# Performance work log

Measured on AMD Instinct MI355X. Metric: run time of the kernel, lower is better.

## Reference

```python
import jax, jax.numpy as jnp
import numpy as np

CNN_DIM = 256
CLASS_NUM = 6
NHOPS = 2
ATT_DIM = 50


def conv1d(x, w, b, pad):
    # x: [B, Cin, L], w: [Cout, Cin, K]
    y = jax.lax.conv_general_dilated(x, w, (1,), [(pad, pad)],
                                     dimension_numbers=('NCH', 'OIH', 'NCH'))
    return y + b[None, :, None]


def setup_inputs() -> dict:
    key = jax.random.key(0)
    ks = jax.random.split(key, 16)
    B, L, V, GE, DE = 8, 128, 30000, 300, 100
    IN = GE + DE
    C = CLASS_NUM
    s = 0.02
    inp = {}
    inp['x'] = jax.random.randint(ks[0], (B, L), 0, V)
    inp['x_len'] = L  # python int, stands in for x_len[0] (max length)
    inp['x_mask'] = jnp.ones((B, L), dtype=jnp.float32)
    inp['gen_table'] = jax.random.normal(ks[1], (V, GE), jnp.float32) * s
    inp['domain_table'] = jax.random.normal(ks[2], (V, DE), jnp.float32) * s
    inp['w1'] = jax.random.normal(ks[3], (128, IN, 5)) * s
    inp['b1'] = jnp.zeros((128,))
    inp['w2'] = jax.random.normal(ks[4], (128, IN, 3)) * s
    inp['b2'] = jnp.zeros((128,))
    inp['w3'] = jax.random.normal(ks[5], (256, 256, 5)) * s
    inp['b3'] = jnp.zeros((256,))
    inp['w4'] = jax.random.normal(ks[6], (256, 256, 5)) * s
    inp['b4'] = jnp.zeros((256,))
    inp['w5'] = jax.random.normal(ks[7], (256, 256, 5)) * s
    inp['b5'] = jnp.zeros((256,))
    inp['wq'] = jax.random.normal(ks[8], (CNN_DIM, ATT_DIM)) * s
    inp['bq'] = jnp.zeros((ATT_DIM,))
    inp['wv'] = jax.random.normal(ks[9], (CNN_DIM, ATT_DIM)) * s
    inp['bv'] = jnp.zeros((ATT_DIM,))
    inp['vv'] = jax.random.normal(ks[10], (ATT_DIM,)) * s
    inp['wf'] = jax.random.normal(ks[11], (2 * CNN_DIM + 3 * C, 2 * CNN_DIM)) * s
    inp['bf'] = jnp.zeros((2 * CNN_DIM,))
    inp['wc'] = jax.random.normal(ks[12], (2 * CNN_DIM, C)) * s
    inp['bc'] = jnp.zeros((C,))
    return inp


def reference(x, x_len, x_mask, gen_table, domain_table,
              w1, b1, w2, b2, w3, b3, w4, b4, w5, b5,
              wq, bq, wv, bv, vv, wf, bf, wc, bc):
    # embeddings (dropout omitted: eval mode)
    emb = jnp.concatenate([gen_table[x], domain_table[x]], axis=2)  # [B,L,400]
    xe = jnp.swapaxes(emb, 1, 2)  # [B,400,L]
    xc = jax.nn.relu(jnp.concatenate([conv1d(xe, w1, b1, 2),
                                      conv1d(xe, w2, b2, 1)], axis=1))
    xc = jax.nn.relu(conv1d(xc, w3, b3, 2))
    xc = jax.nn.relu(conv1d(xc, w4, b4, 2))
    xc = jax.nn.relu(conv1d(xc, w5, b5, 2))
    xc = jnp.swapaxes(xc, 1, 2)[:, :x_len, :]  # [B,L,256]
    mask = x_mask[:, :x_len]
    # perceptron (additive) self-attention: v^T tanh(Wq q_i + Wv v_j)
    q = xc @ wq + bq  # [B,L,50]
    v = xc @ wv + bv  # [B,L,50]
    scores = jnp.tanh(q[:, :, None, :] + v[:, None, :, :]) @ vv  # [B,L,L]
    scores = jnp.where(mask[:, None, :] == 0, -1e9, scores)
    attn = jax.nn.softmax(scores, axis=2)
    merged = jnp.einsum('bij,bjd->bid', attn, xc) * mask[:, :, None]
    xc = xc + merged
    B, L, D = xc.shape
    # grid features: (i,j) -> [h_i, h_j]
    features = jnp.concatenate([
        jnp.broadcast_to(xc[:, :, None, :], (B, L, L, D)),
        jnp.broadcast_to(xc[:, None, :, :], (B, L, L, D))], axis=3)  # [B,L,L,512]
    # upper-triangular validity mask on the grid
    m2 = jnp.triu(mask[:, None, :] * mask[:, :, None])[..., None]  # [B,L,L,1]
    logits = features @ wc + bc  # [B,L,L,C]
    for _ in range(NHOPS):
        probs = logits
        lg = probs * m2
        lm = jnp.maximum(jnp.max(lg, axis=1), jnp.max(lg, axis=2))  # [B,L,C]
        row = jnp.broadcast_to(lm[:, :, None, :], (B, L, L, lm.shape[-1]))
        grid = jnp.concatenate([row, jnp.swapaxes(row, 1, 2)], axis=3)  # [B,L,L,2C]
        features = jnp.concatenate([features, grid, probs], axis=3) @ wf + bf
        logits = features @ wc + bc
    return logits
```

## Files before the change

### kernel.cpp

```cpp
#include <hip/hip_runtime.h>
#include <math.h>

#define LSEQ 128
#define BB 8
#define M_TOK (BB*LSEQ)

typedef __attribute__((ext_vector_type(8))) short short8;
typedef __attribute__((ext_vector_type(4))) float floatx4;

__device__ __forceinline__ unsigned short bf16_rne(float v) {
    union { float f; unsigned u; } a; a.f = v;
    return (unsigned short)((a.u + 0x7fffu + ((a.u >> 16) & 1u)) >> 16);
}
__device__ __forceinline__ float bf16_to_f(unsigned short h) {
    union { unsigned u; float f; } b; b.u = ((unsigned)h) << 16;
    return b.f;
}
__device__ __forceinline__ void split2(float v, unsigned short& h, unsigned short& l) {
    h = bf16_rne(v);
    l = bf16_rne(v - bf16_to_f(h));
}

struct PreArgs {
    const float *w1, *w2, *w3, *w4, *w5;
    unsigned short *B1h, *B1l, *B2h, *B2l, *B3h, *B3l, *B4h, *B4l, *B5h, *B5l;
    const int* x;
    const float* gen;
    const float* dom;
    unsigned short *Eh, *El;
    const float* wf;
    const float* wc;
    float* Wfc;
};
__global__ __launch_bounds__(256) void stage_kernel(PreArgs a) {
    int y = blockIdx.y;
    int tid = threadIdx.x;
    if (y < 3) {
        const float* w = (y == 0) ? a.w3 : (y == 1) ? a.w4 : a.w5;
        unsigned short* dh = (y == 0) ? a.B3h : (y == 1) ? a.B4h : a.B5h;
        unsigned short* dl = (y == 0) ? a.B3l : (y == 1) ? a.B4l : a.B5l;
        int idx = blockIdx.x * 256 + tid;
        int j = idx & 7;
        int n = (idx >> 3) & 255;
        int g = idx >> 11;
        int cg = g & 31, kk = g >> 5;
        int ci = cg * 8 + j;
        float v = w[(n * 256 + ci) * 5 + kk];
        unsigned short h, l; split2(v, h, l);
        dh[idx] = h; dl[idx] = l;
    } else if (y == 3) {
        int idx = blockIdx.x * 256 + tid;
        if (idx >= 5 * 52 * 128 * 8) return;
        int j = idx & 7;
        int n = (idx >> 3) & 127;
        int g = idx >> 10;
        int cg = g % 52, kk = g / 52;
        int ci = cg * 8 + j;
        float v = (ci < 400) ? a.w1[(n * 400 + ci) * 5 + kk] : 0.f;
        unsigned short h, l; split2(v, h, l);
        a.B1h[idx] = h; a.B1l[idx] = l;
    } else if (y == 4) {
        int idx = blockIdx.x * 256 + tid;
        if (idx >= 3 * 52 * 128 * 8) return;
        int j = idx & 7;
        int n = (idx >> 3) & 127;
        int g = idx >> 10;
        int cg = g % 52, kk = g / 52;
        int ci = cg * 8 + j;
        float v = (ci < 400) ? a.w2[(n * 400 + ci) * 3 + kk] : 0.f;
        unsigned short h, l; split2(v, h, l);
        a.B2h[idx] = h; a.B2l[idx] = l;
    } else if (y == 5) {
        int m = blockIdx.x;
        if (m >= M_TOK) return;
        int t = a.x[m];
        for (int c = tid; c < 416; c += 256) {
            float v = (c < 300) ? a.gen[t * 300 + c]
                    : (c < 400) ? a.dom[t * 100 + (c - 300)] : 0.f;
            unsigned short h, l; split2(v, h, l);
            a.Eh[m * 416 + c] = h;
            a.El[m * 416 + c] = l;
        }
    } else {
        int r = blockIdx.x;
        if (r >= 512 || tid >= 64) return;
        int l = tid;
        float p[6] = {0,0,0,0,0,0};
        const float* row = a.wf + r * 512;
        #pragma unroll
        for (int k = 0; k < 8; ++k) {
            int n = l + 64 * k;
            float v = row[n];
            #pragma unroll
            for (int c = 0; c < 6; ++c) p[c] += v * a.wc[n * 6 + c];
        }
        #pragma unroll
        for (int c = 0; c < 6; ++c)
            for (int off = 32; off >= 1; off >>= 1) p[c] += __shfl_xor(p[c], off, 64);
        if (l == 0) {
            #pragma unroll
            for (int c = 0; c < 6; ++c) a.Wfc[r * 6 + c] = p[c];
        }
    }
}

__global__ __launch_bounds__(256) void conv1_mfma(
        const unsigned short* __restrict__ Eh, const unsigned short* __restrict__ El,
        const unsigned short* __restrict__ B1h, const unsigned short* __restrict__ B1l,
        const unsigned short* __restrict__ B2h, const unsigned short* __restrict__ B2l,
        const float* __restrict__ b1, const float* __restrict__ b2,
        unsigned short* __restrict__ Xoh, unsigned short* __restrict__ Xol,
        const float* __restrict__ wf, const float* __restrict__ bf,
        const float* __restrict__ wc, const float* __restrict__ Wfc,
        float* __restrict__ U) {
    __shared__ __align__(16) unsigned short xsh[20 * 424];
    __shared__ __align__(16) unsigned short xsl[20 * 424];
    int by = blockIdx.y;
    int tid = threadIdx.x;
    if (by == 4) {
        if (tid >= 64) return;
        int l = tid;
        for (int i = 0; i < 9; ++i) {
            int r = blockIdx.x + 64 * i;
            if (r >= 531) break;
            const float* row = (r < 530) ? (wf + r * 512) : bf;
            float p[12];
            #pragma unroll
            for (int c = 0; c < 12; ++c) p[c] = 0.f;
            #pragma unroll
            for (int k = 0; k < 8; ++k) {
                int n = l + 64 * k;
                float v = row[n];
                #pragma unroll
                for (int c = 0; c < 6; ++c) {
                    p[c]     += v * wc[n * 6 + c];
                    p[c + 6] += v * Wfc[n * 6 + c];
                }
            }
            #pragma unroll
            for (int c = 0; c < 12; ++c)
                for (int off = 32; off >= 1; off >>= 1) p[c] += __shfl_xor(p[c], off, 64);
            if (l == 0) {
                #pragma unroll
                for (int c = 0; c < 12; ++c) U[r * 12 + c] = p[c];
            }
        }
        return;
    }
    int mt = blockIdx.x;
    int p0 = mt * 16;
    int b = p0 >> 7, l0 = p0 & 127;
    for (int i = tid; i < 2 * 1040; i += 256) {
        int sel = i >= 1040;
        int u2 = sel ? i - 1040 : i;
        int j = u2 / 52, cg = u2 % 52;
        int l = l0 - 2 + j;
        short8 v = {0,0,0,0,0,0,0,0};
        if (l >= 0 && l < 128) {
            const unsigned short* src = (sel ? El : Eh) + (b * 128 + l) * 416 + cg * 8;
            v = *(const short8*)src;
        }
        *(short8*)((sel ? xsl : xsh) + j * 424 + cg * 8) = v;
    }
    __syncthreads();
    int w = tid >> 6, lane = tid & 63;
    int m = lane & 15, q = lane >> 4;
    bool br2 = (by >= 2);
    int n0b = (by & 1) * 64;
    int nB = n0b + w * 16 + m;
    floatx4 acc0 = {0,0,0,0}, acc1 = {0,0,0,0}, acc2 = {0,0,0,0};
    if (!br2) {
        for (int kk = 0; kk < 5; ++kk) {
            const unsigned short* arh = xsh + (m + kk) * 424;
            const unsigned short* arl = xsl + (m + kk) * 424;
            #pragma unroll
            for (int u = 0; u < 13; ++u) {
                short8 ah = *(const short8*)(arh + u * 32 + q * 8);
                short8 al = *(const short8*)(arl + u * 32 + q * 8);
                int boff = (((kk * 52 + u * 4 + q) * 128) + nB) * 8;
                short8 bh = *(const short8*)(B1h + boff);
                short8 bl = *(const short8*)(B1l + boff);
                acc0 = __builtin_amdgcn_mfma_f32_16x16x32_bf16(ah, bh, acc0, 0, 0, 0);
                acc1 = __builtin_amdgcn_mfma_f32_16x16x32_bf16(ah, bl, acc1, 0, 0, 0);
                acc2 = __builtin_amdgcn_mfma_f32_16x16x32_bf16(al, bh, acc2, 0, 0, 0);
            }
        }
    } else {
        for (int kk = 0; kk < 3; ++kk) {
            const unsigned short* arh = xsh + (m + kk + 1) * 424;
            const unsigned short* arl = xsl + (m + kk + 1) * 424;
            #pragma unroll
            for (int u = 0; u < 13; ++u) {
                short8 ah = *(const short8*)(arh + u * 32 + q * 8);
                short8 al = *(const short8*)(arl + u * 32 + q * 8);
                int boff = (((kk * 52 + u * 4 + q) * 128) + nB) * 8;
                short8 bh = *(const short8*)(B2h + boff);
                short8 bl = *(const short8*)(B2l + boff);
                acc0 = __builtin_amdgcn_mfma_f32_16x16x32_bf16(ah, bh, acc0, 0, 0, 0);
                acc1 = __builtin_amdgcn_mfma_f32_16x16x32_bf16(ah, bl, acc1, 0, 0, 0);
                acc2 = __builtin_amdgcn_mfma_f32_16x16x32_bf16(al, bh, acc2, 0, 0, 0);
            }
        }
    }
    __syncthreads();
    float* fl = (float*)xsh;
    #pragma unroll
    for (int reg = 0; reg < 4; ++reg)
        fl[(q * 4 + reg) * 68 + w * 16 + m] = acc0[reg] + acc1[reg] + acc2[reg];
    __syncthreads();
    int ocb = br2 ? 128 + n0b : n0b;
    const float* bias = br2 ? b2 : b1;
    #pragma unroll
    for (int i = 0; i < 4; ++i) {
        int e = tid + 256 * i;
        int mm = e >> 6, nn = e & 63;
        float val = fl[mm * 68 + nn] + bias[n0b + nn];
        val = fmaxf(val, 0.f);
        unsigned short h, l; split2(val, h, l);
        int o = (p0 + mm) * 256 + ocb + nn;
        Xoh[o] = h; Xol[o] = l;
    }
}

__global__ __launch_bounds__(256) void conv256_mfma(
        const unsigned short* __restrict__ Xih, const unsigned short* __restrict__ Xil,
        const unsigned short* __restrict__ Bh, const unsigned short* __restrict__ Bl,
        const float* __restrict__ bias, int outmode,
        unsigned short* __restrict__ Xoh, unsigned short* __restrict__ Xol,
        float* __restrict__ fout) {
    __shared__ __align__(16) unsigned short xsh[20 * 264];
    __shared__ __align__(16) unsigned short xsl[20 * 264];
    int mt = blockIdx.x;
    int p0 = mt * 16;
    int b = p0 >> 7, l0 = p0 & 127;
    int n0 = blockIdx.y * 64;
    int tid = threadIdx.x;
    for (int i = tid; i < 2 * 640; i += 256) {
        int sel = i >= 640;
        int u2 = sel ? i - 640 : i;
        int j = u2 >> 5, cg = u2 & 31;
        int l = l0 - 2 + j;
        short8 v = {0,0,0,0,0,0,0,0};
        if (l >= 0 && l < 128) {
            const unsigned short* src = (sel ? Xil : Xih) + (b * 128 + l) * 256 + cg * 8;
            v = *(const short8*)src;
        }
        *(short8*)((sel ? xsl : xsh) + j * 264 + cg * 8) = v;
    }
    __syncthreads();
    int w = tid >> 6, lane = tid & 63;
    int m = lane & 15, q = lane >> 4;
    int nB = n0 + w * 16 + m;
    floatx4 acc0 = {0,0,0,0}, acc1 = {0,0,0,0}, acc2 = {0,0,0,0};
    for (int kk = 0; kk < 5; ++kk) {
        const unsigned short* arh = xsh + (m + kk) * 264;
        const unsigned short* arl = xsl + (m + kk) * 264;
        #pragma unroll
        for (int u = 0; u < 8; ++u) {
            short8 ah = *(const short8*)(arh + u * 32 + q * 8);
            short8 al = *(const short8*)(arl + u * 32 + q * 8);
            int boff = (((kk * 32 + u * 4 + q) * 256) + nB) * 8;
            short8 bh = *(const short8*)(Bh + boff);
            short8 bl = *(const short8*)(Bl + boff);
            acc0 = __builtin_amdgcn_mfma_f32_16x16x32_bf16(ah, bh, acc0, 0, 0, 0);
        acc1 = __builtin_amdgcn_mfma_f32_16x16x32_bf16(ah, bl, acc1, 0, 0, 0);
            acc2 = __builtin_amdgcn_mfma_f32_16x16x32_bf16(al, bh, acc2, 0, 0, 0);
        }
    }
    __syncthreads();
    float* fl = (float*)xsh;
    #pragma unroll
    for (int reg = 0; reg < 4; ++reg)
        fl[(q * 4 + reg) * 68 + w * 16 + m] = acc0[reg] + acc1[reg] + acc2[reg];
    __syncthreads();
    #pragma unroll
    for (int i = 0; i < 4; ++i) {
        int e = tid + 256 * i;
        int mm = e >> 6, nn = e & 63;
        float val = fl[mm * 68 + nn] + bias[n0 + nn];
        val = fmaxf(val, 0.f);
        int o = (p0 + mm) * 256 + n0 + nn;
        if (outmode == 0) {
            unsigned short h, l; split2(val, h, l);
            Xoh[o] = h; Xol[o] = l;
        } else {
            fout[o] = val;
        }
    }
}

__global__ __launch_bounds__(128) void qv_v2(const float* __restrict__ xc,
        const float* __restrict__ wq, const float* __restrict__ bq,
        const float* __restrict__ wv, const float* __restrict__ bv,
        float* __restrict__ q, float* __restrict__ v) {
    int m = blockIdx.x;
    int tid = threadIdx.x;
    int w = tid >> 6, d = tid & 63;
    if (d >= 50) return;
    const float* W = w ? wv : wq;
    float a = w ? bv[d] : bq[d];
    const float* xm = xc + m * 256;
    #pragma unroll 8
    for (int c = 0; c < 256; ++c) a += xm[c] * W[c * 50 + d];
    (w ? v : q)[m * 50 + d] = a;
}

__global__ __launch_bounds__(256) void attn_v2(const float* __restrict__ xc,
        const float* __restrict__ q, const float* __restrict__ v,
        const float* __restrict__ vv, const float* __restrict__ xmask,
        const float* __restrict__ wc, const float* __restrict__ bc,
        float* __restrict__ xc2, float* __restrict__ f0, float* __restrict__ g0) {
    __shared__ float vs[128 * 50];
    __shared__ float spart[128], aarr[128], xrow[256], qrow[52], vvs[52], red[4];
    int bi = blockIdx.x;
    int b = bi >> 7;
    int tid = threadIdx.x;
    for (int idx = tid; idx < 128 * 50; idx += 256) vs[idx] = v[b * 6400 + idx];
    if (tid < 50) { qrow[tid] = q[bi * 50 + tid]; vvs[tid] = vv[tid]; }
    __syncthreads();
    int j = tid & 127, half = tid >> 7;
    int d0 = half * 25;
    const float* vj = vs + j * 50 + d0;
    float s = 0.f;
    #pragma unroll
    for (int d = 0; d < 25; ++d) {
        float x = qrow[d0 + d] + vj[d];
        float e = __expf(2.f * x);
        s += (1.f - 2.f / (e + 1.f)) * vvs[d0 + d];
    }
    if (half) spart[j] = s;
    __syncthreads();
    float stot = 0.f;
    if (!half) {
        stot = s + spart[j];
        if (xmask[b * LSEQ + j] == 0.f) stot = -1e9f;
    }
    if (tid < 128) {
        float m = stot;
        #pragma unroll
        for (int off = 32; off >= 1; off >>= 1) m = fmaxf(m, __shfl_xor(m, off, 64));
        if ((tid & 63) == 0) red[tid >> 6] = m;
    }
    __syncthreads();
    float mx = fmaxf(red[0], red[1]);
    float e = 0.f;
    if (tid < 128) {
        e = __expf(stot - mx);
        float su = e;
        #pragma unroll
        for (int off = 32; off >= 1; off >>= 1) su += __shfl_xor(su, off, 64);
        if ((tid & 63) == 0) red[2 + (tid >> 6)] = su;
    }
    __syncthreads();
    float denom = red[2] + red[3];
    if (tid < 128) aarr[j] = e / denom;
    __syncthreads();
    float maskI = xmask[bi];
    const float* xcb = xc + b * LSEQ * 256;
    float acc = 0.f;
    #pragma unroll 8
    for (int jj = 0; jj < 128; ++jj) acc += aarr[jj] * xcb[jj * 256 + tid];
    float val = xc[bi * 256 + tid] + acc * maskI;
    xc2[bi * 256 + tid] = val;
    xrow[tid] = val;
    __syncthreads();
    int grp = tid >> 4, l16 = tid & 15;
    if (grp < 12) {
        int c = grp % 6, gsel = grp / 6;
        const float* wcc = wc + gsel * 256 * 6 + c;
        float a = 0.f;
        #pragma unroll
        for (int ch = l16; ch < 256; ch += 16) a += xrow[ch] * wcc[ch * 6];
        #pragma unroll
        for (int off = 8; off >= 1; off >>= 1) a += __shfl_down(a, off, 16);
        if (l16 == 0) {
            if (gsel == 0) f0[bi * 6 + c] = a + bc[c];
            else           g0[bi * 6 + c] = a;
        }
    }
}

__global__ __launch_bounds__(128) void lm_scan_v3(const float* __restrict__ f,
        const float* __restrict__ g, int stride, float* __restrict__ lm) {
    __shared__ float sf[128], sg[128];
    int bc = blockIdx.x;
    int b = bc / 6, c = bc - b * 6;
    int p = threadIdx.x;
    float fv = f[(b * LSEQ + p) * stride + c];
    float gv = g[(b * LSEQ + p) * stride + c];
    sf[p] = fv; sg[p] = gv;
    __syncthreads();
    float pf = fv, sgx = gv;
    #pragma unroll
    for (int off = 1; off < 128; off <<= 1) {
        float a = (p >= off) ? sf[p - off] : -INFINITY;
        float d = (p + off < 128) ? sg[p + off] : -INFINITY;
        __syncthreads();
        pf = fmaxf(pf, a); sgx = fmaxf(sgx, d);
        sf[p] = pf; sg[p] = sgx;
        __syncthreads();
    }
    float M1 = pf + gv;
    if (p < LSEQ - 1) M1 = fmaxf(M1, 0.f);
    float M2 = fv + sgx;
    if (p > 0) M2 = fmaxf(M2, 0.f);
    lm[(b * LSEQ + p) * 6 + c] = fmaxf(M1, M2);
}

__global__ __launch_bounds__(64) void hopfold_kernel(const float* __restrict__ xc2,
        const float* __restrict__ U, const float* __restrict__ lm0,
        const float* __restrict__ f0, const float* __restrict__ g0,
        const float* __restrict__ bc,
        float* __restrict__ outF, float* __restrict__ outG) {
    int m = blockIdx.x;
    int y = blockIdx.y;
    int tid = threadIdx.x;
    const float* Urows = U + (y ? 256 : 0) * 12;
    float p[12];
    #pragma unroll
    for (int c = 0; c < 12; ++c) p[c] = 0.f;
    for (int k = tid; k < 256; k += 64) {
        float a = xc2[m * 256 + k];
        const float* ur = Urows + k * 12;
        #pragma unroll
        for (int c = 0; c < 12; ++c) p[c] += a * ur[c];
    }
    #pragma unroll
    for (int c = 0; c < 12; ++c)
        for (int off = 32; off >= 1; off >>= 1) p[c] += __shfl_xor(p[c], off, 64);
    if (tid == 0) {
        const float* Bb = U + (y ? 518 : 512) * 12;
        const float* Db = U + 524 * 12;
        const float* fg = y ? g0 : f0;
        float* out = y ? outG : outF;
        float lmv[6], fgv[6];
        #pragma unroll
        for (int j = 0; j < 6; ++j) { lmv[j] = lm0[m * 6 + j]; fgv[j] = fg[m * 6 + j]; }
        #pragma unroll
        for (int c = 0; c < 12; ++c) {
            float s = p[c];
            #pragma unroll
            for (int j = 0; j < 6; ++j) s += lmv[j] * Bb[j * 12 + c] + fgv[j] * Db[j * 12 + c];
            if (!y) { s += U[530 * 12 + c]; if (c < 6) s += bc[c]; }
            out[m * 12 + c] = s;
        }
    }
}

__global__ __launch_bounds__(128) void f2g2_kernel(const float* __restrict__ f1phi,
        const float* __restrict__ g1gam, const float* __restrict__ lm1,
        const float* __restrict__ U, const float* __restrict__ bc,
        float* __restrict__ f2, float* __restrict__ g2) {
    __shared__ float Us[19 * 12], bcs[6];
    int tid = threadIdx.x;
    for (int i = tid; i < 19 * 12; i += 128) Us[i] = U[512 * 12 + i];
    if (tid < 6) bcs[tid] = bc[tid];
    __syncthreads();
    int m = blockIdx.x * 128 + tid;
    float lmv[6], f1v[6], g1v[6];
    #pragma unroll
    for (int j = 0; j < 6; ++j) {
        lmv[j] = lm1[m * 6 + j];
        f1v[j] = f1phi[m * 12 + j];
        g1v[j] = g1gam[m * 12 + j];
    }
    #pragma unroll
    for (int c = 0; c < 6; ++c) {
        float sf = f1phi[m * 12 + 6 + c] + Us[18 * 12 + c] + bcs[c];
        float sg = g1gam[m * 12 + 6 + c];
        #pragma unroll
        for (int j = 0; j < 6; ++j) {
            sf += lmv[j] * Us[j * 12 + c]       + f1v[j] * Us[(12 + j) * 12 + c];
            sg += lmv[j] * Us[(6 + j) * 12 + c] + g1v[j] * Us[(12 + j) * 12 + c];
        }
        f2[m * 6 + c] = sf;
        g2[m * 6 + c] = sg;
    }
}

__global__ __launch_bounds__(256) void writeout_kernel(const float* __restrict__ f2,
        const float* __restrict__ g2, float* __restrict__ out) {
    int idx = blockIdx.x * 256 + threadIdx.x;
    int c = idx % 6;
    int r = idx / 6;
    int j = r & 127;
    int bi = r >> 7;
    int b = bi >> 7;
    out[idx] = f2[bi * 6 + c] + g2[(b * LSEQ + j) * 6 + c];
}

extern "C" void kernel_launch(void* const* d_in, const int* in_sizes, int n_in,
                              void* d_out, int out_size, void* d_ws, size_t ws_size,
                              hipStream_t stream) {
    const int*   x     = (const int*)d_in[0];
    const float* xmask = (const float*)d_in[2];
    const float* gen   = (const float*)d_in[3];
    const float* dom   = (const float*)d_in[4];
    const float* w1    = (const float*)d_in[5];
    const float* b1    = (const float*)d_in[6];
    const float* w2    = (const float*)d_in[7];
    const float* b2    = (const float*)d_in[8];
    const float* w3    = (const float*)d_in[9];
    const float* b3    = (const float*)d_in[10];
    const float* w4    = (const float*)d_in[11];
    const float* b4    = (const float*)d_in[12];
    const float* w5    = (const float*)d_in[13];
    const float* b5    = (const float*)d_in[14];
    const float* wq    = (const float*)d_in[15];
    const float* bq    = (const float*)d_in[16];
    const float* wv    = (const float*)d_in[17];
    const float* bv    = (const float*)d_in[18];
    const float* vv    = (const float*)d_in[19];
    const float* wf    = (const float*)d_in[20];
    const float* bf    = (const float*)d_in[21];
    const float* wc    = (const float*)d_in[22];
    const float* bc    = (const float*)d_in[23];

    float* fb = (float*)d_ws;
    float* bufB  = fb;
    float* xc2   = bufB  + 262144;
    float* qb    = xc2   + 262144;
    float* vb    = qb    + 51200;
    float* Wfc   = vb    + 51200;
    float* U     = Wfc   + 3072;
    float* f0    = U     + 6376;
    float* g0    = f0    + 6144;
    float* lm0   = g0    + 6144;
    float* lm1   = lm0   + 6144;
    float* f1phi = lm1   + 6144;
    float* g1gam = f1phi + 12288;
    float* f2    = g1gam + 12288;
    float* g2    = f2    + 6144;
    unsigned short* sb = (unsigned short*)(g2 + 6144 + 32);
    unsigned short* Eh  = sb;             sb += 425984;
    unsigned short* El  = sb;             sb += 425984;
    unsigned short* B1h = sb;             sb += 266240;
    unsigned short* B1l = sb;             sb += 266240;
    unsigned short* B2h = sb;             sb += 159744;
    unsigned short* B2l = sb;             sb += 159744;
    unsigned short* B3h = sb;             sb += 327680;
    unsigned short* B3l = sb;             sb += 327680;
    unsigned short* B4h = sb;             sb += 327680;
    unsigned short* B4l = sb;             sb += 327680;
    unsigned short* B5h = sb;             sb += 327680;
    unsigned short* B5l = sb;             sb += 327680;
    unsigned short* X3h = sb;             sb += 262144;
    unsigned short* X3l = sb;             sb += 262144;
    unsigned short* X4h = sb;             sb += 262144;
    unsigned short* X4l = sb;             sb += 262144;

    PreArgs pa;
    pa.w1 = w1; pa.w2 = w2; pa.w3 = w3; pa.w4 = w4; pa.w5 = w5;
    pa.B1h = B1h; pa.B1l = B1l; pa.B2h = B2h; pa.B2l = B2l;
    pa.B3h = B3h; pa.B3l = B3l; pa.B4h = B4h; pa.B4l = B4l;
    pa.B5h = B5h; pa.B5l = B5l;
    pa.x = x; pa.gen = gen; pa.dom = dom; pa.Eh = Eh; pa.El = El;
    pa.wf = wf; pa.wc = wc; pa.Wfc = Wfc;
    stage_kernel<<<dim3(1280, 7), 256, 0, stream>>>(pa);

    conv1_mfma<<<dim3(64, 5), 256, 0, stream>>>(Eh, El, B1h, B1l, B2h, B2l, b1, b2,
                                                X3h, X3l, wf, bf, wc, Wfc, U);
    conv256_mfma<<<dim3(64, 4), 256, 0, stream>>>(X3h, X3l, B3h, B3l, b3, 0,
                                                  X4h, X4l, nullptr);
    conv256_mfma<<<dim3(64, 4), 256, 0, stream>>>(X4h, X4l, B4h, B4l, b4, 0,
                                                  X3h, X3l, nullptr);
    conv256_mfma<<<dim3(64, 4), 256, 0, stream>>>(X3h, X3l, B5h, B5l, b5, 1,
                                                  nullptr, nullptr, bufB);

    qv_v2<<<M_TOK, 128, 0, stream>>>(bufB, wq, bq, wv, bv, qb, vb);
    attn_v2<<<M_TOK, 256, 0, stream>>>(bufB, qb, vb, vv, xmask, wc, bc, xc2, f0, g0);

    lm_scan_v3<<<48, 128, 0, stream>>>(f0, g0, 6, lm0);
    hopfold_kernel<<<dim3(M_TOK, 2), 64, 0, stream>>>(xc2, U, lm0, f0, g0, bc, f1phi, g1gam);
    lm_scan_v3<<<48, 128, 0, stream>>>(f1phi, g1gam, 12, lm1);
    f2g2_kernel<<<8, 128, 0, stream>>>(f1phi, g1gam, lm1, U, bc, f2, g2);

    writeout_kernel<<<(BB*LSEQ*LSEQ*6)/256, 256, 0, stream>>>(f2, g2, (float*)d_out);
}
```

Before: 240.1 us.

## Fuse hop scans, folds and writeout into two kernels; enlarge conv M-tile

```diff
diff --git a/kernel.cpp b/kernel.cpp
--- a/kernel.cpp
+++ b/kernel.cpp
@@ -228,16 +228,16 @@
         const float* __restrict__ bias, int outmode,
         unsigned short* __restrict__ Xoh, unsigned short* __restrict__ Xol,
         float* __restrict__ fout) {
-    __shared__ __align__(16) unsigned short xsh[20 * 264];
-    __shared__ __align__(16) unsigned short xsl[20 * 264];
+    __shared__ __align__(16) unsigned short xsh[36 * 264];
+    __shared__ __align__(16) unsigned short xsl[36 * 264];
     int mt = blockIdx.x;
-    int p0 = mt * 16;
+    int p0 = mt * 32;
     int b = p0 >> 7, l0 = p0 & 127;
     int n0 = blockIdx.y * 64;
     int tid = threadIdx.x;
-    for (int i = tid; i < 2 * 640; i += 256) {
-        int sel = i >= 640;
-        int u2 = sel ? i - 640 : i;
+    for (int i = tid; i < 2 * 1152; i += 256) {
+        int sel = i >= 1152;
+        int u2 = sel ? i - 1152 : i;
         int j = u2 >> 5, cg = u2 & 31;
         int l = l0 - 2 + j;
         short8 v = {0,0,0,0,0,0,0,0};
@@ -251,30 +251,40 @@
     int w = tid >> 6, lane = tid & 63;
     int m = lane & 15, q = lane >> 4;
     int nB = n0 + w * 16 + m;
-    floatx4 acc0 = {0,0,0,0}, acc1 = {0,0,0,0}, acc2 = {0,0,0,0};
+    floatx4 acc0a = {0,0,0,0}, acc1a = {0,0,0,0}, acc2a = {0,0,0,0};
+    floatx4 acc0b = {0,0,0,0}, acc1b = {0,0,0,0}, acc2b = {0,0,0,0};
     for (int kk = 0; kk < 5; ++kk) {
-        const unsigned short* arh = xsh + (m + kk) * 264;
-        const unsigned short* arl = xsl + (m + kk) * 264;
+        const unsigned short* arh0 = xsh + (m + kk) * 264;
+        const unsigned short* arl0 = xsl + (m + kk) * 264;
+        const unsigned short* arh1 = arh0 + 16 * 264;
+        const unsigned short* arl1 = arl0 + 16 * 264;
         #pragma unroll
         for (int u = 0; u < 8; ++u) {
-            short8 ah = *(const short8*)(arh + u * 32 + q * 8);
-            short8 al = *(const short8*)(arl + u * 32 + q * 8);
+            short8 ah0 = *(const short8*)(arh0 + u * 32 + q * 8);
+            short8 al0 = *(const short8*)(arl0 + u * 32 + q * 8);
+            short8 ah1 = *(const short8*)(arh1 + u * 32 + q * 8);
+            short8 al1 = *(const short8*)(arl1 + u * 32 + q * 8);
             int boff = (((kk * 32 + u * 4 + q) * 256) + nB) * 8;
             short8 bh = *(const short8*)(Bh + boff);
             short8 bl = *(const short8*)(Bl + boff);
-            acc0 = __builtin_amdgcn_mfma_f32_16x16x32_bf16(ah, bh, acc0, 0, 0, 0);
-        acc1 = __builtin_amdgcn_mfma_f32_16x16x32_bf16(ah, bl, acc1, 0, 0, 0);
-            acc2 = __builtin_amdgcn_mfma_f32_16x16x32_bf16(al, bh, acc2, 0, 0, 0);
+            acc0a = __builtin_amdgcn_mfma_f32_16x16x32_bf16(ah0, bh, acc0a, 0, 0, 0);
+            acc1a = __builtin_amdgcn_mfma_f32_16x16x32_bf16(ah0, bl, acc1a, 0, 0, 0);
+            acc2a = __builtin_amdgcn_mfma_f32_16x16x32_bf16(al0, bh, acc2a, 0, 0, 0);
+            acc0b = __builtin_amdgcn_mfma_f32_16x16x32_bf16(ah1, bh, acc0b, 0, 0, 0);
+            acc1b = __builtin_amdgcn_mfma_f32_16x16x32_bf16(ah1, bl, acc1b, 0, 0, 0);
+            acc2b = __builtin_amdgcn_mfma_f32_16x16x32_bf16(al1, bh, acc2b, 0, 0, 0);
         }
     }
     __syncthreads();
     float* fl = (float*)xsh;
     #pragma unroll
-    for (int reg = 0; reg < 4; ++reg)
-        fl[(q * 4 + reg) * 68 + w * 16 + m] = acc0[reg] + acc1[reg] + acc2[reg];
-    __syncthreads();
-    #pragma unroll
-    for (int i = 0; i < 4; ++i) {
+    for (int reg = 0; reg < 4; ++reg) {
+        fl[(q * 4 + reg) * 68 + w * 16 + m]        = acc0a[reg] + acc1a[reg] + acc2a[reg];
+        fl[(16 + q * 4 + reg) * 68 + w * 16 + m]   = acc0b[reg] + acc1b[reg] + acc2b[reg];
+    }
+    __syncthreads();
+    #pragma unroll
+    for (int i = 0; i < 8; ++i) {
         int e = tid + 256 * i;
         int mm = e >> 6, nn = e & 63;
         float val = fl[mm * 68 + nn] + bias[n0 + nn];
@@ -380,113 +390,196 @@
     }
 }
 
-__global__ __launch_bounds__(128) void lm_scan_v3(const float* __restrict__ f,
-        const float* __restrict__ g, int stride, float* __restrict__ lm) {
-    __shared__ float sf[128], sg[128];
-    int bc = blockIdx.x;
-    int b = bc / 6, c = bc - b * 6;
-    int p = threadIdx.x;
-    float fv = f[(b * LSEQ + p) * stride + c];
-    float gv = g[(b * LSEQ + p) * stride + c];
-    sf[p] = fv; sg[p] = gv;
-    __syncthreads();
-    float pf = fv, sgx = gv;
+__global__ __launch_bounds__(256) void hop1_kernel(const float* __restrict__ xc2,
+        const float* __restrict__ U, const float* __restrict__ f0,
+        const float* __restrict__ g0, const float* __restrict__ bc,
+        float* __restrict__ outF, float* __restrict__ outG) {
+    __shared__ float sf0[768], sg0[768], sfw[768], sgw[768], lms[768];
+    int b = blockIdx.x >> 4, grp = blockIdx.x & 15;
+    int tid = threadIdx.x;
+    for (int i = tid; i < 768; i += 256) {
+        sf0[i] = f0[b * 768 + i];
+        sg0[i] = g0[b * 768 + i];
+    }
+    __syncthreads();
+    int p = tid;
+    float fv[6], gv[6], pf[6], sx[6];
+    if (p < 128) {
+        #pragma unroll
+        for (int c = 0; c < 6; ++c) {
+            fv[c] = sf0[p * 6 + c]; gv[c] = sg0[p * 6 + c];
+            pf[c] = fv[c]; sx[c] = gv[c];
+            sfw[p * 6 + c] = fv[c]; sgw[p * 6 + c] = gv[c];
+        }
+    }
+    __syncthreads();
     #pragma unroll
     for (int off = 1; off < 128; off <<= 1) {
-        float a = (p >= off) ? sf[p - off] : -INFINITY;
-        float d = (p + off < 128) ? sg[p + off] : -INFINITY;
+        float av[6], dv[6];
+        if (p < 128) {
+            #pragma unroll
+            for (int c = 0; c < 6; ++c) {
+                av[c] = (p >= off) ? sfw[(p - off) * 6 + c] : -INFINITY;
+                dv[c] = (p + off < 128) ? sgw[(p + off) * 6 + c] : -INFINITY;
+            }
+        }
         __syncthreads();
-        pf = fmaxf(pf, a); sgx = fmaxf(sgx, d);
-        sf[p] = pf; sg[p] = sgx;
+        if (p < 128) {
+            #pragma unroll
+            for (int c = 0; c < 6; ++c) {
+                pf[c] = fmaxf(pf[c], av[c]); sx[c] = fmaxf(sx[c], dv[c]);
+                sfw[p * 6 + c] = pf[c]; sgw[p * 6 + c] = sx[c];
+            }
+        }
         __syncthreads();
     }
-    float M1 = pf + gv;
-    if (p < LSEQ - 1) M1 = fmaxf(M1, 0.f);
-    float M2 = fv + sgx;
-    if (p > 0) M2 = fmaxf(M2, 0.f);
-    lm[(b * LSEQ + p) * 6 + c] = fmaxf(M1, M2);
-}
-
-__global__ __launch_bounds__(64) void hopfold_kernel(const float* __restrict__ xc2,
-        const float* __restrict__ U, const float* __restrict__ lm0,
-        const float* __restrict__ f0, const float* __restrict__ g0,
-        const float* __restrict__ bc,
-        float* __restrict__ outF, float* __restrict__ outG) {
-    int m = blockIdx.x;
-    int y = blockIdx.y;
+    if (p < 128) {
+        #pragma unroll
+        for (int c = 0; c < 6; ++c) {
+            float M1 = pf[c] + gv[c];
+            if (p < LSEQ - 1) M1 = fmaxf(M1, 0.f);
+            float M2 = fv[c] + sx[c];
+            if (p > 0) M2 = fmaxf(M2, 0.f);
+            lms[p * 6 + c] = fmaxf(M1, M2);
+        }
+    }
+    __syncthreads();
+    int t = tid >> 5, lane = tid & 31;
+    int ptok = grp * 8 + t;
+    int m = b * 128 + ptok;
+    float p24[24];
+    #pragma unroll
+    for (int c = 0; c < 24; ++c) p24[c] = 0.f;
+    const floatx4* U4 = (const floatx4*)U;
+    const float* xm = xc2 + m * 256;
+    #pragma unroll
+    for (int kk = 0; kk < 8; ++kk) {
+        int k = lane + 32 * kk;
+        float a = xm[k];
+        floatx4 u0[3], u1[3];
+        #pragma unroll
+        for (int t3 = 0; t3 < 3; ++t3) { u0[t3] = U4[k * 3 + t3]; u1[t3] = U4[(256 + k) * 3 + t3]; }
+        #pragma unroll
+        for (int t3 = 0; t3 < 3; ++t3)
+            #pragma unroll
+            for (int qd = 0; qd < 4; ++qd) {
+                p24[t3 * 4 + qd]      += a * u0[t3][qd];
+                p24[12 + t3 * 4 + qd] += a * u1[t3][qd];
+            }
+    }
+    #pragma unroll
+    for (int c = 0; c < 24; ++c)
+        for (int off = 16; off >= 1; off >>= 1) p24[c] += __shfl_xor(p24[c], off, 32);
+    if (lane < 12) {
+        int c = lane;
+        float s0 = p24[c], s1 = p24[12 + c];
+        #pragma unroll
+        for (int jj = 0; jj < 6; ++jj) {
+            float lmv = lms[ptok * 6 + jj];
+            float f0v = sf0[ptok * 6 + jj];
+            float g0v = sg0[ptok * 6 + jj];
+            float dbv = U[(524 + jj) * 12 + c];
+            s0 += lmv * U[(512 + jj) * 12 + c] + f0v * dbv;
+            s1 += lmv * U[(518 + jj) * 12 + c] + g0v * dbv;
+        }
+        s0 += U[530 * 12 + c];
+        if (c < 6) s0 += bc[c];
+        outF[m * 12 + c] = s0;
+        outG[m * 12 + c] = s1;
+    }
+}
+
+__global__ __launch_bounds__(256) void hop2_kernel(const float* __restrict__ f1phi,
+        const float* __restrict__ g1gam, const float* __restrict__ U,
+        const float* __restrict__ bc, float* __restrict__ out) {
+    __shared__ float f1s[128 * 12], g1s[128 * 12];
+    __shared__ float sfw[768], sgw[768], lm1s[768], f2s[768], g2s[768];
+    __shared__ float Us[228], bcs[6];
+    int b = blockIdx.x >> 4, ys = blockIdx.x & 15;
     int tid = threadIdx.x;
-    const float* Urows = U + (y ? 256 : 0) * 12;
-    float p[12];
-    #pragma unroll
-    for (int c = 0; c < 12; ++c) p[c] = 0.f;
-    for (int k = tid; k < 256; k += 64) {
-        float a = xc2[m * 256 + k];
-        const float* ur = Urows + k * 12;
-        #pragma unroll
-        for (int c = 0; c < 12; ++c) p[c] += a * ur[c];
-    }
-    #pragma unroll
-    for (int c = 0; c < 12; ++c)
-        for (int off = 32; off >= 1; off >>= 1) p[c] += __shfl_xor(p[c], off, 64);
-    if (tid == 0) {
-        const float* Bb = U + (y ? 518 : 512) * 12;
-        const float* Db = U + 524 * 12;
-        const float* fg = y ? g0 : f0;
-        float* out = y ? outG : outF;
-        float lmv[6], fgv[6];
-        #pragma unroll
-        for (int j = 0; j < 6; ++j) { lmv[j] = lm0[m * 6 + j]; fgv[j] = fg[m * 6 + j]; }
-        #pragma unroll
-        for (int c = 0; c < 12; ++c) {
-            float s = p[c];
-            #pragma unroll
-            for (int j = 0; j < 6; ++j) s += lmv[j] * Bb[j * 12 + c] + fgv[j] * Db[j * 12 + c];
-            if (!y) { s += U[530 * 12 + c]; if (c < 6) s += bc[c]; }
-            out[m * 12 + c] = s;
-        }
-    }
-}
-
-__global__ __launch_bounds__(128) void f2g2_kernel(const float* __restrict__ f1phi,
-        const float* __restrict__ g1gam, const float* __restrict__ lm1,
-        const float* __restrict__ U, const float* __restrict__ bc,
-        float* __restrict__ f2, float* __restrict__ g2) {
-    __shared__ float Us[19 * 12], bcs[6];
-    int tid = threadIdx.x;
-    for (int i = tid; i < 19 * 12; i += 128) Us[i] = U[512 * 12 + i];
+    for (int i = tid; i < 1536; i += 256) {
+        f1s[i] = f1phi[b * 1536 + i];
+        g1s[i] = g1gam[b * 1536 + i];
+    }
+    if (tid < 228) Us[tid] = U[512 * 12 + tid];
     if (tid < 6) bcs[tid] = bc[tid];
     __syncthreads();
-    int m = blockIdx.x * 128 + tid;
-    float lmv[6], f1v[6], g1v[6];
-    #pragma unroll
-    for (int j = 0; j < 6; ++j) {
-        lmv[j] = lm1[m * 6 + j];
-        f1v[j] = f1phi[m * 12 + j];
-        g1v[j] = g1gam[m * 12 + j];
-    }
-    #pragma unroll
-    for (int c = 0; c < 6; ++c) {
-        float sf = f1phi[m * 12 + 6 + c] + Us[18 * 12 + c] + bcs[c];
-        float sg = g1gam[m * 12 + 6 + c];
-        #pragma unroll
-        for (int j = 0; j < 6; ++j) {
-            sf += lmv[j] * Us[j * 12 + c]       + f1v[j] * Us[(12 + j) * 12 + c];
-            sg += lmv[j] * Us[(6 + j) * 12 + c] + g1v[j] * Us[(12 + j) * 12 + c];
-        }
-        f2[m * 6 + c] = sf;
-        g2[m * 6 + c] = sg;
-    }
-}
-
-__global__ __launch_bounds__(256) void writeout_kernel(const float* __restrict__ f2,
-        const float* __restrict__ g2, float* __restrict__ out) {
-    int idx = blockIdx.x * 256 + threadIdx.x;
-    int c = idx % 6;
-    int r = idx / 6;
-    int j = r & 127;
-    int bi = r >> 7;
-    int b = bi >> 7;
-    out[idx] = f2[bi * 6 + c] + g2[(b * LSEQ + j) * 6 + c];
+    int p = tid;
+    float fv[6], gv[6], pf[6], sx[6];
+    if (p < 128) {
+        #pragma unroll
+        for (int c = 0; c < 6; ++c) {
+            fv[c] = f1s[p * 12 + c]; gv[c] = g1s[p * 12 + c];
+            pf[c] = fv[c]; sx[c] = gv[c];
+            sfw[p * 6 + c] = fv[c]; sgw[p * 6 + c] = gv[c];
+        }
+    }
+    __syncthreads();
+    #pragma unroll
+    for (int off = 1; off < 128; off <<= 1) {
+        float av[6], dv[6];
+        if (p < 128) {
+            #pragma unroll
+            for (int c = 0; c < 6; ++c) {
+                av[c] = (p >= off) ? sfw[(p - off) * 6 + c] : -INFINITY;
+                dv[c] = (p + off < 128) ? sgw[(p + off) * 6 + c] : -INFINITY;
+            }
+        }
+        __syncthreads();
+        if (p < 128) {
+            #pragma unroll
+            for (int c = 0; c < 6; ++c) {
+                pf[c] = fmaxf(pf[c], av[c]); sx[c] = fmaxf(sx[c], dv[c]);
+                sfw[p * 6 + c] = pf[c]; sgw[p * 6 + c] = sx[c];
+            }
+        }
+        __syncthreads();
+    }
+    if (p < 128) {
+        #pragma unroll
+        for (int c = 0; c < 6; ++c) {
+            float M1 = pf[c] + gv[c];
+            if (p < LSEQ - 1) M1 = fmaxf(M1, 0.f);
+            float M2 = fv[c] + sx[c];
+            if (p > 0) M2 = fmaxf(M2, 0.f);
+            lm1s[p * 6 + c] = fmaxf(M1, M2);
+        }
+    }
+    __syncthreads();
+    if (p < 128) {
+        float lmv[6], f1v[6], g1v[6];
+        #pragma unroll
+        for (int jj = 0; jj < 6; ++jj) {
+            lmv[jj] = lm1s[p * 6 + jj];
+            f1v[jj] = f1s[p * 12 + jj];
+            g1v[jj] = g1s[p * 12 + jj];
+        }
+        #pragma unroll
+        for (int c = 0; c < 6; ++c) {
+            float sf = f1s[p * 12 + 6 + c] + Us[18 * 12 + c] + bcs[c];
+            float sg = g1s[p * 12 + 6 + c];
+            #pragma unroll
+            for (int jj = 0; jj < 6; ++jj) {
+                sf += lmv[jj] * Us[jj * 12 + c]       + f1v[jj] * Us[(12 + jj) * 12 + c];
+                sg += lmv[jj] * Us[(6 + jj) * 12 + c] + g1v[jj] * Us[(12 + jj) * 12 + c];
+            }
+            f2s[p * 6 + c] = sf;
+            g2s[p * 6 + c] = sg;
+        }
+    }
+    __syncthreads();
+    floatx4* out4 = (floatx4*)out;
+    for (int e = tid; e < 1536; e += 256) {
+        int i = e / 12, part = e - i * 12;
+        floatx4 wv;
+        #pragma unroll
+        for (int qd = 0; qd < 4; ++qd) {
+            int idx = part * 4 + qd;
+            int jj = idx / 6, c = idx - jj * 6;
+            wv[qd] = f2s[i * 6 + c] + g2s[(ys * 8 + jj) * 6 + c];
+        }
+        out4[(b * 128 + i) * 192 + ys * 12 + part] = wv;
+    }
 }
 
 extern "C" void kernel_launch(void* const* d_in, const int* in_sizes, int n_in,
@@ -531,6 +624,7 @@
     float* g1gam = f1phi + 12288;
     float* f2    = g1gam + 12288;
     float* g2    = f2    + 6144;
+    (void)lm0; (void)lm1; (void)f2;
     unsigned short* sb = (unsigned short*)(g2 + 6144 + 32);
     unsigned short* Eh  = sb;             sb += 425984;
     unsigned short* El  = sb;             sb += 425984;
@@ -560,20 +654,16 @@
 
     conv1_mfma<<<dim3(64, 5), 256, 0, stream>>>(Eh, El, B1h, B1l, B2h, B2l, b1, b2,
                                                 X3h, X3l, wf, bf, wc, Wfc, U);
-    conv256_mfma<<<dim3(64, 4), 256, 0, stream>>>(X3h, X3l, B3h, B3l, b3, 0,
+    conv256_mfma<<<dim3(32, 4), 256, 0, stream>>>(X3h, X3l, B3h, B3l, b3, 0,
                                                   X4h, X4l, nullptr);
-    conv256_mfma<<<dim3(64, 4), 256, 0, stream>>>(X4h, X4l, B4h, B4l, b4, 0,
+    conv256_mfma<<<dim3(32, 4), 256, 0, stream>>>(X4h, X4l, B4h, B4l, b4, 0,
                                                   X3h, X3l, nullptr);
-    conv256_mfma<<<dim3(64, 4), 256, 0, stream>>>(X3h, X3l, B5h, B5l, b5, 1,
+    conv256_mfma<<<dim3(32, 4), 256, 0, stream>>>(X3h, X3l, B5h, B5l, b5, 1,
                                                   nullptr, nullptr, bufB);
 
     qv_v2<<<M_TOK, 128, 0, stream>>>(bufB, wq, bq, wv, bv, qb, vb);
     attn_v2<<<M_TOK, 256, 0, stream>>>(bufB, qb, vb, vv, xmask, wc, bc, xc2, f0, g0);
 
-    lm_scan_v3<<<48, 128, 0, stream>>>(f0, g0, 6, lm0);
-    hopfold_kernel<<<dim3(M_TOK, 2), 64, 0, stream>>>(xc2, U, lm0, f0, g0, bc, f1phi, g1gam);
-    lm_scan_v3<<<48, 128, 0, stream>>>(f1phi, g1gam, 12, lm1);
-    f2g2_kernel<<<8, 128, 0, stream>>>(f1phi, g1gam, lm1, U, bc, f2, g2);
-
-    writeout_kernel<<<(BB*LSEQ*LSEQ*6)/256, 256, 0, stream>>>(f2, g2, (float*)d_out);
-}
+    hop1_kernel<<<128, 256, 0, stream>>>(xc2, U, f0, g0, bc, f1phi, g1gam);
+    hop2_kernel<<<128, 256, 0, stream>>>(f1phi, g1gam, U, bc, (float*)d_out);
+}
```

After: 254.9 us. 6.2% more time.
